# Performance work log

Hardware: AMD Instinct MI355X
Metric: run time of the kernel (lower is better)

Reference implementation:

```python
import jax, jax.numpy as jnp
import numpy as np

B, Tu, Tm, Tz = 32, 128, 128, 32
V, H, E = 10000, 512, 128
S = E + H  # state_size


def setup_inputs() -> dict:
    key = jax.random.key(0)
    ks = jax.random.split(key, 24)
    u_input = jax.random.randint(ks[0], (B, Tu), 0, V)
    m_input = jax.random.randint(ks[1], (B, Tm), 0, V)
    pv_z_idx = jax.random.randint(ks[2], (B, Tz), 0, V)
    inp = {
        'u_input': u_input,
        'u_input_1hot': jax.nn.one_hot(u_input, V, dtype=jnp.float32),
        'u_hiddens': jax.random.normal(ks[3], (B, Tu, H), jnp.float32),
        'm_input': m_input,
        'm_input_1hot': jax.nn.one_hot(m_input, V, dtype=jnp.float32),
        'm_hiddens': jax.random.normal(ks[4], (B, Tm, H), jnp.float32),
        'pv_z_prob': jax.nn.softmax(jax.random.normal(ks[5], (B, Tz, V), jnp.float32), axis=-1),
        'pv_z_hidden': jax.random.normal(ks[6], (B, Tz, H), jnp.float32),
        'pv_z_idx': pv_z_idx,
        'emb_zt': jax.random.normal(ks[7], (B, 1, E), jnp.float32),
        'last_hidden': jax.random.normal(ks[8], (1, B, H), jnp.float32),
        # Attn params (concat attention: v . tanh(W [h; enc]))
        'W_attn': jax.random.normal(ks[9], (H, 2 * H), jnp.float32) * 0.02,
        'b_attn': jnp.zeros((H,), jnp.float32),
        'v_attn': jax.random.normal(ks[10], (H,), jnp.float32) * 0.05,
        # GRU params (torch gate order r,z,n)
        'W_ih': jax.random.normal(ks[11], (3 * H, S), jnp.float32) * 0.02,
        'W_hh': jax.random.normal(ks[12], (3 * H, H), jnp.float32) * 0.02,
        'b_ih': jnp.zeros((3 * H,), jnp.float32),
        'b_hh': jnp.zeros((3 * H,), jnp.float32),
        # generation / copy-score projections
        'W_gen': jax.random.normal(ks[13], (V, S), jnp.float32) * 0.02,
        'b_gen': jnp.zeros((V,), jnp.float32),
        'W_cpu': jax.random.normal(ks[14], (S, H), jnp.float32) * 0.02,
        'b_cpu': jnp.zeros((S,), jnp.float32),
        'W_cpm': jax.random.normal(ks[15], (S, H), jnp.float32) * 0.02,
        'b_cpm': jnp.zeros((S,), jnp.float32),
        'W_cppz': jax.random.normal(ks[16], (S, H), jnp.float32) * 0.02,
        'b_cppz': jnp.zeros((S,), jnp.float32),
    }
    return inp


def reference(u_input, u_input_1hot, u_hiddens, m_input, m_input_1hot, m_hiddens,
              pv_z_prob, pv_z_hidden, pv_z_idx, emb_zt, last_hidden,
              W_attn, b_attn, v_attn, W_ih, W_hh, b_ih, b_hh,
              W_gen, b_gen, W_cpu, b_cpu, W_cpm, b_cpm, W_cppz, b_cppz):
    Bv, Tuv, Vv = u_input_1hot.shape
    Tmv = m_hiddens.shape[1]
    t_input = emb_zt  # [B,1,E] (enable_selc_read=False)

    # ---- concat attention over [u; m; pv_z] hiddens ----
    enc = jnp.concatenate([u_hiddens, m_hiddens, pv_z_hidden], axis=1)  # [B,T,H]
    h0 = jnp.transpose(last_hidden, (1, 0, 2))  # [B,1,H]
    hid_rep = jnp.broadcast_to(h0, (Bv, enc.shape[1], h0.shape[2]))
    energy = jnp.tanh(jnp.einsum('bth,gh->btg', jnp.concatenate([hid_rep, enc], axis=2), W_attn) + b_attn)
    attn_w = jax.nn.softmax(jnp.einsum('bth,h->bt', energy, v_attn), axis=1)
    context = jnp.einsum('bt,bth->bh', attn_w, enc)[:, None, :]  # [B,1,H]

    # ---- single GRU step (torch gate order r,z,n) ----
    x = jnp.concatenate([t_input, context], axis=2)[:, 0, :]  # [B,E+H]
    h = h0[:, 0, :]
    gi = x @ W_ih.T + b_ih
    gh = h @ W_hh.T + b_hh
    i_r, i_z, i_n = jnp.split(gi, 3, axis=1)
    h_r, h_z, h_n = jnp.split(gh, 3, axis=1)
    r = jax.nn.sigmoid(i_r + h_r)
    z = jax.nn.sigmoid(i_z + h_z)
    n = jnp.tanh(i_n + r * h_n)
    h_new = (1.0 - z) * n + z * h  # [B,H]
    gru_out = h_new[:, None, :]
    last_hidden_new = h_new[None, :, :]

    # ---- generation + copy scores ----
    st = jnp.concatenate([h_new, t_input[:, 0, :]], axis=1)  # [B,E+H]
    score_g = st @ W_gen.T + b_gen  # [B,V]
    sc_u = jnp.einsum('bts,bs->bt', jnp.tanh(jnp.einsum('bth,sh->bts', u_hiddens, W_cpu) + b_cpu), st)
    sc_m = jnp.einsum('bts,bs->bt', jnp.tanh(jnp.einsum('bth,sh->bts', m_hiddens, W_cpm) + b_cpm), st)
    sc_pz = jnp.einsum('bts,bs->bt', jnp.tanh(jnp.einsum('bth,sh->bts', pv_z_hidden, W_cppz) + b_cppz), st)
    probs = jax.nn.softmax(jnp.concatenate([score_g, sc_u, sc_m, sc_pz], axis=1), axis=1)

    p_g = probs[:, :Vv]
    p_u = probs[:, Vv:Vv + Tuv]
    p_m = probs[:, Vv + Tuv:Vv + Tuv + Tmv]
    p_pz = probs[:, Vv + Tuv + Tmv:]
    prob_out = (p_g
                + jnp.einsum('bt,btv->bv', p_u, u_input_1hot)
                + jnp.einsum('bt,btv->bv', p_m, m_input_1hot)
                + jnp.einsum('bt,btv->bv', p_pz, pv_z_prob))
    return (prob_out, last_hidden_new, gru_out)
```

## Files before the change

### kernel.cpp

```cpp
#include <hip/hip_runtime.h>
#include <math.h>

#define B   32
#define TU  128
#define TM  128
#define TZ  32
#define TENC 288
#define V   10000
#define H   512
#define E   128
#define S   640
#define G3  1536
#define NLOG (V + TENC)

#define WS_Q      0
#define WS_SCORE  (WS_Q + B*H)
#define WS_CTX    (WS_SCORE + B*TENC)
#define WS_GI     (WS_CTX + B*H)
#define WS_GH     (WS_GI + B*G3)
#define WS_ST     (WS_GH + B*G3)
#define WS_LOGIT  (WS_ST + B*S)
#define WS_PCOPY  (WS_LOGIT + B*NLOG)
#define WS_F_TOTAL (WS_PCOPY + B*TENC)

#define BF_WA2  0
#define BF_WCP  (BF_WA2 + 512*512)
#define BF_ENC  (BF_WCP + 3*640*512)
#define BF_ST   (BF_ENC + B*TENC*H)
#define BF_TANH (BF_ST + B*S)

typedef __attribute__((ext_vector_type(8))) short bf16x8_t;
typedef __attribute__((ext_vector_type(4))) float f32x4_t;
typedef __attribute__((ext_vector_type(16))) float f32x16_t;

__device__ __forceinline__ float fast_tanh(float x) {
    return 1.f - 2.f / (__expf(2.f * x) + 1.f);
}

__device__ __forceinline__ unsigned short f2bf(float x) {
    unsigned int u = __float_as_uint(x);
    u += 0x7fffu + ((u >> 16) & 1u);
    return (unsigned short)(u >> 16);
}

__device__ __forceinline__ float bf2f(unsigned short u) {
    return __uint_as_float(((unsigned int)u) << 16);
}

__device__ __forceinline__ bf16x8_t cvt8(const float* p) {
    float4 a = *(const float4*)(p);
    float4 b = *(const float4*)(p + 4);
    bf16x8_t r;
    r[0] = (short)f2bf(a.x); r[1] = (short)f2bf(a.y);
    r[2] = (short)f2bf(a.z); r[3] = (short)f2bf(a.w);
    r[4] = (short)f2bf(b.x); r[5] = (short)f2bf(b.y);
    r[6] = (short)f2bf(b.z); r[7] = (short)f2bf(b.w);
    return r;
}

__device__ __forceinline__ const float* enc_row(const float* u, const float* m,
                                                const float* pz, int b, int t) {
    if (t < TU) return u + ((size_t)b * TU + t) * H;
    if (t < TU + TM) return m + ((size_t)b * TM + (t - TU)) * H;
    return pz + ((size_t)b * TZ + (t - TU - TM)) * H;
}

#define CVT_WA2_END  65536
#define CVT_TOTAL    (CVT_WA2_END + 3*81920)
#define CVTE_TOTAL   (B * TENC * 128)
#define CVT_ALL      (CVT_TOTAL + CVTE_TOTAL)
#define NMV          112
__global__ __launch_bounds__(256) void k_prep(const float* __restrict__ W_attn,
                                              const float* __restrict__ W_cpu,
                                              const float* __restrict__ W_cpm,
                                              const float* __restrict__ W_cppz,
                                              const float* __restrict__ u_h,
                                              const float* __restrict__ m_h,
                                              const float* __restrict__ pz_h,
                                              const float* __restrict__ last_h,
                                              const float* __restrict__ emb,
                                              const float* __restrict__ W_hh,
                                              const float* __restrict__ W_ih,
                                              const float* __restrict__ b_attn,
                                              const float* __restrict__ b_hh,
                                              const float* __restrict__ b_ih,
                                              float* __restrict__ ws,
                                              unsigned short* __restrict__ bf) {
    int blk = blockIdx.x, tid = threadIdx.x;
    __shared__ float redmv[4][64][16];
    if (blk < NMV) {
        int wave = tid >> 6, lane = tid & 63;
        int m = lane & 31, khalf = lane >> 5;
        f32x16_t acc = {};
        int n;
        if (blk < 16) {
            n = blk * 32 + m;
            const float* aptr = last_h + (size_t)m * H + khalf * 8;
            const float* bptr = W_attn + (size_t)n * 1024 + khalf * 8;
            for (int k0 = wave * 128; k0 < wave * 128 + 128; k0 += 16)
                acc = __builtin_amdgcn_mfma_f32_32x32x16_bf16(cvt8(aptr + k0),
                                                              cvt8(bptr + k0), acc, 0, 0, 0);
        } else if (blk < 64) {
            n = (blk - 16) * 32 + m;
            const float* aptr = last_h + (size_t)m * H + khalf * 8;
            const float* bptr = W_hh + (size_t)n * H + khalf * 8;
            for (int k0 = wave * 128; k0 < wave * 128 + 128; k0 += 16)
                acc = __builtin_amdgcn_mfma_f32_32x32x16_bf16(cvt8(aptr + k0),
                                                              cvt8(bptr + k0), acc, 0, 0, 0);
        } else {
            n = (blk - 64) * 32 + m;
            const float* aptr = emb + (size_t)m * E + khalf * 8;
            const float* bptr = W_ih + (size_t)n * S + khalf * 8;
            for (int k0 = wave * 32; k0 < wave * 32 + 32; k0 += 16)
                acc = __builtin_amdgcn_mfma_f32_32x32x16_bf16(cvt8(aptr + k0),
                                                              cvt8(bptr + k0), acc, 0, 0, 0);
        }
#pragma unroll
        for (int r = 0; r < 16; ++r) redmv[wave][lane][r] = acc[r];
        __syncthreads();
        if (wave == 0) {
#pragma unroll
            for (int r = 0; r < 16; ++r) {
                float v = redmv[0][lane][r] + redmv[1][lane][r] +
                          redmv[2][lane][r] + redmv[3][lane][r];
                int row = (r & 3) + 8 * (r >> 2) + 4 * khalf;
                if (blk < 16)      ws[WS_Q  + row * H  + n] = v + b_attn[n];
                else if (blk < 64) ws[WS_GH + row * G3 + n] = v + b_hh[n];
                else               ws[WS_GI + row * G3 + n] = v + b_ih[n];
            }
        }
        return;
    }
    int idx = (blk - NMV) * 256 + tid;
    if (idx >= CVT_ALL) return;
    const float* src;
    unsigned short* dst;
    if (idx < CVT_WA2_END) {
        int g = idx >> 7, c4 = idx & 127;
        int k = c4 * 4, kt = k >> 5, kin = k & 31;
        src = W_attn + (size_t)g * 1024 + 512 + k;
        dst = bf + BF_WA2 + kt * (512 * 32) + g * 32 + kin;
    } else if (idx < CVT_TOTAL) {
        int r = idx - CVT_WA2_END;
        int seg = r / 81920, q = r % 81920;
        int s = q >> 7, c4 = q & 127;
        int k = c4 * 4, kt = k >> 5, kin = k & 31;
        const float* s0 = (seg == 0) ? W_cpu : (seg == 1) ? W_cpm : W_cppz;
        src = s0 + (size_t)s * 512 + k;
        dst = bf + BF_WCP + seg * 327680 + kt * (640 * 32) + s * 32 + kin;
    } else {
        int e = idx - CVT_TOTAL;
        int b = e / (TENC * 128);
        int r = e % (TENC * 128);
        int t = r >> 7, c4 = r & 127;
        int k = c4 * 4, kt = k >> 5, kin = k & 31;
        src = enc_row(u_h, m_h, pz_h, b, t) + k;
        dst = bf + BF_ENC + (((size_t)b * 16 + kt) * TENC + t) * 32 + kin;
    }
    float4 v = *(const float4*)src;
    ushort4 o;
    o.x = f2bf(v.x); o.y = f2bf(v.y); o.z = f2bf(v.z); o.w = f2bf(v.w);
    *(ushort4*)dst = o;
}

__global__ __launch_bounds__(256) void k_enc_mfma(const unsigned short* __restrict__ bf,
                                                  const float* __restrict__ v_attn,
                                                  const float* __restrict__ b_cpu,
                                                  const float* __restrict__ b_cpm,
                                                  const float* __restrict__ b_cppz,
                                                  float* __restrict__ ws,
                                                  unsigned short* __restrict__ bft) {
    __shared__ __attribute__((aligned(16))) unsigned short lds_w[640 * 32];
    __shared__ __attribute__((aligned(16))) unsigned short lds_a[32 * 32];
    __shared__ float red[4][32];
    int blk = blockIdx.x;
    int typeC = (blk >= 288);
    int idx = typeC ? blk - 288 : blk;
    int b = idx / 9, t0 = (idx % 9) * 32;
    int tid = threadIdx.x, wave = tid >> 6, lane = tid & 63;
    int n16 = lane & 15, quad = lane >> 4;
    const unsigned short* asrc0 =
        bf + BF_ENC + (((size_t)b * 16) * TENC + t0) * 32;
    if (!typeC) {
        f32x4_t acc[2][8];
#pragma unroll
        for (int tl = 0; tl < 2; ++tl)
#pragma unroll
            for (int j = 0; j < 8; ++j) acc[tl][j] = (f32x4_t){0.f, 0.f, 0.f, 0.f};
        for (int kt = 0; kt < 16; ++kt) {
            const unsigned short* wsrc = bf + BF_WA2 + (size_t)kt * (512 * 32);
#pragma unroll
            for (int c = 0; c < 8; ++c) {
                int u = (c * 256 + tid) * 8;
                *(bf16x8_t*)&lds_w[u] = *(const bf16x8_t*)&wsrc[u];
            }
            if (tid < 128) {
                int u = tid * 8;
                *(bf16x8_t*)&lds_a[u] =
                    *(const bf16x8_t*)&asrc0[(size_t)kt * TENC * 32 + u];
            }
            __syncthreads();
            bf16x8_t a0 = *(const bf16x8_t*)&lds_a[n16 * 32 + quad * 8];
            bf16x8_t a1 = *(const bf16x8_t*)&lds_a[(n16 + 16) * 32 + quad * 8];
#pragma unroll
            for (int j = 0; j < 8; ++j) {
                bf16x8_t bb = *(const bf16x8_t*)
                    &lds_w[((wave * 8 + j) * 16 + n16) * 32 + quad * 8];
                acc[0][j] = __builtin_amdgcn_mfma_f32_16x16x32_bf16(a0, bb, acc[0][j], 0, 0, 0);
                acc[1][j] = __builtin_amdgcn_mfma_f32_16x16x32_bf16(a1, bb, acc[1][j], 0, 0, 0);
            }
            __syncthreads();
        }
        float sval[2][4] = {{0.f, 0.f, 0.f, 0.f}, {0.f, 0.f, 0.f, 0.f}};
#pragma unroll
        for (int j = 0; j < 8; ++j) {
            int g = (wave * 8 + j) * 16 + n16;
            float q = ws[WS_Q + b * H + g];
            float va = v_attn[g];
#pragma unroll
            for (int tl = 0; tl < 2; ++tl)
#pragma unroll
                for (int r = 0; r < 4; ++r)
                    sval[tl][r] += fast_tanh(acc[tl][j][r] + q) * va;
        }
#pragma unroll
        for (int tl = 0; tl < 2; ++tl)
#pragma unroll
            for (int r = 0; r < 4; ++r)
#pragma unroll
                for (int off = 8; off > 0; off >>= 1)
                    sval[tl][r] += __shfl_down(sval[tl][r], off, 64);
        if (n16 == 0)
#pragma unroll
            for (int tl = 0; tl < 2; ++tl)
#pragma unroll
                for (int r = 0; r < 4; ++r)
                    red[wave][tl * 16 + quad * 4 + r] = sval[tl][r];
        __syncthreads();
        if (tid < 32)
            ws[WS_SCORE + b * TENC + t0 + tid] =
                red[0][tid] + red[1][tid] + red[2][tid] + red[3][tid];
    } else {
        int seg = (t0 < TU) ? 0 : (t0 < TU + TM) ? 1 : 2;
        const float* bias = (seg == 0) ? b_cpu : (seg == 1) ? b_cpm : b_cppz;
        f32x4_t acc[2][10];
#pragma unroll
        for (int tl = 0; tl < 2; ++tl)
#pragma unroll
            for (int j = 0; j < 10; ++j) acc[tl][j] = (f32x4_t){0.f, 0.f, 0.f, 0.f};
        for (int kt = 0; kt < 16; ++kt) {
            const unsigned short* wsrc =
                bf + BF_WCP + seg * 327680 + (size_t)kt * (640 * 32);
#pragma unroll
            for (int c = 0; c < 10; ++c) {
                int u = (c * 256 + tid) * 8;
                *(bf16x8_t*)&lds_w[u] = *(const bf16x8_t*)&wsrc[u];
            }
            if (tid < 128) {
                int u = tid * 8;
                *(bf16x8_t*)&lds_a[u] =
                    *(const bf16x8_t*)&asrc0[(size_t)kt * TENC * 32 + u];
            }
            __syncthreads();
            bf16x8_t a0 = *(const bf16x8_t*)&lds_a[n16 * 32 + quad * 8];
            bf16x8_t a1 = *(const bf16x8_t*)&lds_a[(n16 + 16) * 32 + quad * 8];
#pragma unroll
            for (int j = 0; j < 10; ++j) {
                bf16x8_t bb = *(const bf16x8_t*)
                    &lds_w[((wave * 10 + j) * 16 + n16) * 32 + quad * 8];
                acc[0][j] = __builtin_amdgcn_mfma_f32_16x16x32_bf16(a0, bb, acc[0][j], 0, 0, 0);
                acc[1][j] = __builtin_amdgcn_mfma_f32_16x16x32_bf16(a1, bb, acc[1][j], 0, 0, 0);
            }
            __syncthreads();
        }
#pragma unroll
        for (int j = 0; j < 10; ++j) {
            int s = (wave * 10 + j) * 16 + n16;
            float bi = bias[s];
#pragma unroll
            for (int tl = 0; tl < 2; ++tl)
#pragma unroll
                for (int r = 0; r < 4; ++r) {
                    int t = t0 + tl * 16 + quad * 4 + r;
                    bft[BF_TANH + ((size_t)b * TENC + t) * S + s] =
                        f2bf(fast_tanh(acc[tl][j][r] + bi));
                }
        }
    }
}

__global__ __launch_bounds__(256) void k_softmax_ctx(const unsigned short* __restrict__ bf,
                                                     float* __restrict__ ws) {
    int b = blockIdx.x, tid = threadIdx.x;
    __shared__ float wsm[TENC];
    __shared__ float red1[4], red2[4];
    float local = -1e30f;
    for (int t = tid; t < TENC; t += 256) {
        float s = ws[WS_SCORE + b * TENC + t];
        wsm[t] = s;
        local = fmaxf(local, s);
    }
    int lane = tid & 63, wv = tid >> 6;
    for (int off = 32; off > 0; off >>= 1) local = fmaxf(local, __shfl_down(local, off, 64));
    if (lane == 0) red1[wv] = local;
    __syncthreads();
    float mx = fmaxf(fmaxf(red1[0], red1[1]), fmaxf(red1[2], red1[3]));
    float ls = 0.f;
    for (int t = tid; t < TENC; t += 256) {
        float e = __expf(wsm[t] - mx);
        wsm[t] = e;
        ls += e;
    }
    for (int off = 32; off > 0; off >>= 1) ls += __shfl_down(ls, off, 64);
    if (lane == 0) red2[wv] = ls;
    __syncthreads();
    float inv = 1.f / (red2[0] + red2[1] + red2[2] + red2[3]);

    int h2 = tid * 2;
    int kt = h2 >> 5, hin = h2 & 31;
    const unsigned short* ep = bf + BF_ENC + ((size_t)b * 16 + kt) * TENC * 32 + hin;
    float a00 = 0.f, a01 = 0.f, a10 = 0.f, a11 = 0.f;
#pragma unroll 2
    for (int t = 0; t < TENC; t += 2) {
        ushort2 v0 = *(const ushort2*)(ep + (size_t)t * 32);
        ushort2 v1 = *(const ushort2*)(ep + (size_t)(t + 1) * 32);
        float w0 = wsm[t], w1 = wsm[t + 1];
        a00 += w0 * bf2f(v0.x); a10 += w0 * bf2f(v0.y);
        a01 += w1 * bf2f(v1.x); a11 += w1 * bf2f(v1.y);
    }
    ws[WS_CTX + b * H + h2]     = (a00 + a01) * inv;
    ws[WS_CTX + b * H + h2 + 1] = (a10 + a11) * inv;
}

__global__ __launch_bounds__(256) void k_gru_ctx(const float* __restrict__ W_ih,
                                                 float* __restrict__ ws) {
    int blk = blockIdx.x, tid = threadIdx.x;
    __shared__ float redmv[4][64][16];
    int wave = tid >> 6, lane = tid & 63;
    int m = lane & 31, khalf = lane >> 5;
    int n = blk * 32 + m;
    const float* aptr = ws + WS_CTX + (size_t)m * H + khalf * 8;
    const float* bptr = W_ih + (size_t)n * S + E + khalf * 8;
    f32x16_t acc = {};
    for (int k0 = wave * 128; k0 < wave * 128 + 128; k0 += 16)
        acc = __builtin_amdgcn_mfma_f32_32x32x16_bf16(cvt8(aptr + k0),
                                                      cvt8(bptr + k0), acc, 0, 0, 0);
#pragma unroll
    for (int r = 0; r < 16; ++r) redmv[wave][lane][r] = acc[r];
    __syncthreads();
    if (wave == 0) {
#pragma unroll
        for (int r = 0; r < 16; ++r) {
            float v = redmv[0][lane][r] + redmv[1][lane][r] +
                      redmv[2][lane][r] + redmv[3][lane][r];
            int row = (r & 3) + 8 * (r >> 2) + 4 * khalf;
            ws[WS_GI + row * G3 + n] += v;
        }
    }
}

__global__ __launch_bounds__(256) void k_combine(const float* __restrict__ emb,
                                                 const float* __restrict__ last_hidden,
                                                 float* __restrict__ ws,
                                                 unsigned short* __restrict__ bf,
                                                 float* __restrict__ out) {
    int i = blockIdx.x * 256 + threadIdx.x;
    int b = i >> 9, h = i & 511;
    float gi_r = ws[WS_GI + b * G3 + h];
    float gi_z = ws[WS_GI + b * G3 + H + h];
    float gi_n = ws[WS_GI + b * G3 + 2 * H + h];
    float gh_r = ws[WS_GH + b * G3 + h];
    float gh_z = ws[WS_GH + b * G3 + H + h];
    float gh_n = ws[WS_GH + b * G3 + 2 * H + h];
    float rr = 1.f / (1.f + __expf(-(gi_r + gh_r)));
    float zz = 1.f / (1.f + __expf(-(gi_z + gh_z)));
    float nn = fast_tanh(gi_n + rr * gh_n);
    float hp = last_hidden[b * H + h];
    float hn = (1.f - zz) * nn + zz * hp;
    out[V * B + b * H + h] = hn;
    out[V * B + B * H + b * H + h] = hn;
    ws[WS_ST + b * S + h] = hn;
    bf[BF_ST + b * S + h] = f2bf(hn);
    if (h < E) {
        float ev = emb[b * E + h];
        ws[WS_ST + b * S + H + h] = ev;
        bf[BF_ST + b * S + H + h] = f2bf(ev);
    }
}

__global__ __launch_bounds__(256) void k_logits(const unsigned short* __restrict__ bf,
                                                const float* __restrict__ W_gen,
                                                const float* __restrict__ b_gen,
                                                float* __restrict__ ws) {
    int blk = blockIdx.x, tid = threadIdx.x;
    __shared__ float shmem[4 * 64 * 16];
    int wave = tid >> 6, lane = tid & 63;
    if (blk < 576) {
        int b = blk / 18, t0 = (blk % 18) * 16;
        float* st_s = shmem;
        for (int i = tid; i < S; i += 256) st_s[i] = ws[WS_ST + b * S + i];
        __syncthreads();
#pragma unroll
        for (int tl = 0; tl < 4; ++tl) {
            int t = t0 + wave * 4 + tl;
            const unsigned short* row = bf + BF_TANH + ((size_t)b * TENC + t) * S;
            float acc = 0.f;
#pragma unroll
            for (int i = 0; i < 10; ++i) {
                int s = lane + 64 * i;
                acc += bf2f(row[s]) * st_s[s];
            }
            for (int off = 32; off > 0; off >>= 1) acc += __shfl_down(acc, off, 64);
            if (lane == 0) ws[WS_LOGIT + (size_t)b * NLOG + V + t] = acc;
        }
    } else {
        float (*redmv)[64][16] = (float (*)[64][16])shmem;
        int m = lane & 31, khalf = lane >> 5;
        int n = (blk - 576) * 32 + m;
        int nr = (n < V) ? n : (V - 1);
        const unsigned short* aptr = bf + BF_ST + (size_t)m * S + khalf * 8;
        const float* bptr = W_gen + (size_t)nr * S + khalf * 8;
        f32x16_t acc = {};
        for (int k0 = wave * 160; k0 < wave * 160 + 160; k0 += 16)
            acc = __builtin_amdgcn_mfma_f32_32x32x16_bf16(*(const bf16x8_t*)(aptr + k0),
                                                          cvt8(bptr + k0), acc, 0, 0, 0);
#pragma unroll
        for (int r = 0; r < 16; ++r) redmv[wave][lane][r] = acc[r];
        __syncthreads();
        if (wave == 0 && n < V) {
            float bg = b_gen[n];
#pragma unroll
            for (int r = 0; r < 16; ++r) {
                float v = redmv[0][lane][r] + redmv[1][lane][r] +
                          redmv[2][lane][r] + redmv[3][lane][r];
                int row = (r & 3) + 8 * (r >> 2) + 4 * khalf;
                ws[WS_LOGIT + (size_t)row * NLOG + n] = v + bg;
            }
        }
    }
}

__global__ __launch_bounds__(512) void k_softmax_scatter(const int* __restrict__ u_in,
                                                         const int* __restrict__ m_in,
                                                         float* __restrict__ ws,
                                                         float* __restrict__ out) {
    int b = blockIdx.x, tid = threadIdx.x;
    __shared__ float red1[8], red2[8];
    __shared__ float ex[NLOG];
    const float* lg = ws + WS_LOGIT + (size_t)b * NLOG;
    float mx = -1e30f;
    for (int i = tid; i < NLOG; i += 512) {
        float v = lg[i];
        ex[i] = v;
        mx = fmaxf(mx, v);
    }
    int lane = tid & 63, wv = tid >> 6;
    for (int off = 32; off > 0; off >>= 1) mx = fmaxf(mx, __shfl_down(mx, off, 64));
    if (lane == 0) red1[wv] = mx;
    __syncthreads();
    mx = red1[0];
#pragma unroll
    for (int w = 1; w < 8; ++w) mx = fmaxf(mx, red1[w]);
    float sm = 0.f;
    for (int i = tid; i < NLOG; i += 512) {
        float e = __expf(ex[i] - mx);
        ex[i] = e;
        sm += e;
    }
    for (int off = 32; off > 0; off >>= 1) sm += __shfl_down(sm, off, 64);
    if (lane == 0) red2[wv] = sm;
    __syncthreads();
    sm = red2[0];
#pragma unroll
    for (int w = 1; w < 8; ++w) sm += red2[w];
    float inv = 1.f / sm;
    for (int i = tid; i < V; i += 512) out[b * V + i] = ex[i] * inv;
    __syncthreads();
    if (tid < TU + TM) {
        int idx = (tid < TU) ? u_in[b * TU + tid] : m_in[b * TM + (tid - TU)];
        atomicAdd(&out[(size_t)b * V + idx], ex[V + tid] * inv);
    } else if (tid < TENC) {
        ws[WS_PCOPY + b * TENC + tid] = ex[V + tid] * inv;
    }
}

__global__ __launch_bounds__(256) void k_pv(const float* __restrict__ pvp,
                                            const float* __restrict__ ws,
                                            float* __restrict__ out) {
    int b = blockIdx.y;
    int v = blockIdx.x * 256 + threadIdx.x;
    __shared__ float p[TZ];
    if (threadIdx.x < TZ) p[threadIdx.x] = ws[WS_PCOPY + b * TENC + TU + TM + threadIdx.x];
    __syncthreads();
    if (v >= V) return;
    float acc = 0.f;
#pragma unroll 4
    for (int t = 0; t < TZ; ++t) acc += p[t] * pvp[((size_t)b * TZ + t) * V + v];
    out[(size_t)b * V + v] += acc;
}

extern "C" void kernel_launch(void* const* d_in, const int* in_sizes, int n_in,
                              void* d_out, int out_size, void* d_ws, size_t ws_size,
                              hipStream_t stream) {
    const int*   u_input   = (const int*)d_in[0];
    const float* u_h       = (const float*)d_in[2];
    const int*   m_input   = (const int*)d_in[3];
    const float* m_h       = (const float*)d_in[5];
    const float* pv_prob   = (const float*)d_in[6];
    const float* pz_h      = (const float*)d_in[7];
    const float* emb       = (const float*)d_in[9];
    const float* last_h    = (const float*)d_in[10];
    const float* W_attn    = (const float*)d_in[11];
    const float* b_attn    = (const float*)d_in[12];
    const float* v_attn    = (const float*)d_in[13];
    const float* W_ih      = (const float*)d_in[14];
    const float* W_hh      = (const float*)d_in[15];
    const float* b_ih      = (const float*)d_in[16];
    const float* b_hh      = (const float*)d_in[17];
    const float* W_gen     = (const float*)d_in[18];
    const float* b_gen     = (const float*)d_in[19];
    const float* W_cpu     = (const float*)d_in[20];
    const float* b_cpu     = (const float*)d_in[21];
    const float* W_cpm     = (const float*)d_in[22];
    const float* b_cpm     = (const float*)d_in[23];
    const float* W_cppz    = (const float*)d_in[24];
    const float* b_cppz    = (const float*)d_in[25];
    float* ws  = (float*)d_ws;
    unsigned short* bf = (unsigned short*)(ws + WS_F_TOTAL);
    float* out = (float*)d_out;

    hipLaunchKernelGGL(k_prep, dim3(NMV + CVT_ALL / 256), dim3(256), 0, stream,
                       W_attn, W_cpu, W_cpm, W_cppz, u_h, m_h, pz_h,
                       last_h, emb, W_hh, W_ih, b_attn, b_hh, b_ih, ws, bf);
    hipLaunchKernelGGL(k_enc_mfma, dim3(576), dim3(256), 0, stream,
                       bf, v_attn, b_cpu, b_cpm, b_cppz, ws, bf);
    hipLaunchKernelGGL(k_softmax_ctx, dim3(B), dim3(256), 0, stream, bf, ws);
    hipLaunchKernelGGL(k_gru_ctx, dim3(48), dim3(256), 0, stream, W_ih, ws);
    hipLaunchKernelGGL(k_combine, dim3(64), dim3(256), 0, stream, emb, last_h, ws, bf, out);
    hipLaunchKernelGGL(k_logits, dim3(576 + 313), dim3(256), 0, stream, bf, W_gen, b_gen, ws);
    hipLaunchKernelGGL(k_softmax_scatter, dim3(B), dim3(512), 0, stream,
                       u_input, m_input, ws, out);
    hipLaunchKernelGGL(k_pv, dim3(40, B), dim3(256), 0, stream, pv_prob, ws, out);
}
```

Before: 468.1 us.

## Register-prefetch next K-tile in attention/copy GEMM and unroll pv loop more

```diff
diff --git a/kernel.cpp b/kernel.cpp
--- a/kernel.cpp
+++ b/kernel.cpp
@@ -182,24 +182,46 @@
     const unsigned short* asrc0 =
         bf + BF_ENC + (((size_t)b * 16) * TENC + t0) * 32;
     if (!typeC) {
+        bf16x8_t rw0, rw1, rw2, rw3, rw4, rw5, rw6, rw7, ra;
+        const unsigned short* wb = bf + BF_WA2;
+        rw0 = *(const bf16x8_t*)&wb[(0 * 256 + tid) * 8];
+        rw1 = *(const bf16x8_t*)&wb[(1 * 256 + tid) * 8];
+        rw2 = *(const bf16x8_t*)&wb[(2 * 256 + tid) * 8];
+        rw3 = *(const bf16x8_t*)&wb[(3 * 256 + tid) * 8];
+        rw4 = *(const bf16x8_t*)&wb[(4 * 256 + tid) * 8];
+        rw5 = *(const bf16x8_t*)&wb[(5 * 256 + tid) * 8];
+        rw6 = *(const bf16x8_t*)&wb[(6 * 256 + tid) * 8];
+        rw7 = *(const bf16x8_t*)&wb[(7 * 256 + tid) * 8];
+        if (tid < 128) ra = *(const bf16x8_t*)&asrc0[tid * 8];
+        *(bf16x8_t*)&lds_w[(0 * 256 + tid) * 8] = rw0;
+        *(bf16x8_t*)&lds_w[(1 * 256 + tid) * 8] = rw1;
+        *(bf16x8_t*)&lds_w[(2 * 256 + tid) * 8] = rw2;
+        *(bf16x8_t*)&lds_w[(3 * 256 + tid) * 8] = rw3;
+        *(bf16x8_t*)&lds_w[(4 * 256 + tid) * 8] = rw4;
+        *(bf16x8_t*)&lds_w[(5 * 256 + tid) * 8] = rw5;
+        *(bf16x8_t*)&lds_w[(6 * 256 + tid) * 8] = rw6;
+        *(bf16x8_t*)&lds_w[(7 * 256 + tid) * 8] = rw7;
+        if (tid < 128) *(bf16x8_t*)&lds_a[tid * 8] = ra;
+        __syncthreads();
         f32x4_t acc[2][8];
 #pragma unroll
         for (int tl = 0; tl < 2; ++tl)
 #pragma unroll
             for (int j = 0; j < 8; ++j) acc[tl][j] = (f32x4_t){0.f, 0.f, 0.f, 0.f};
         for (int kt = 0; kt < 16; ++kt) {
-            const unsigned short* wsrc = bf + BF_WA2 + (size_t)kt * (512 * 32);
-#pragma unroll
-            for (int c = 0; c < 8; ++c) {
-                int u = (c * 256 + tid) * 8;
-                *(bf16x8_t*)&lds_w[u] = *(const bf16x8_t*)&wsrc[u];
-            }
-            if (tid < 128) {
-                int u = tid * 8;
-                *(bf16x8_t*)&lds_a[u] =
-                    *(const bf16x8_t*)&asrc0[(size_t)kt * TENC * 32 + u];
-            }
-            __syncthreads();
+            if (kt < 15) {
+                const unsigned short* wsrc = wb + (size_t)(kt + 1) * (512 * 32);
+                rw0 = *(const bf16x8_t*)&wsrc[(0 * 256 + tid) * 8];
+                rw1 = *(const bf16x8_t*)&wsrc[(1 * 256 + tid) * 8];
+                rw2 = *(const bf16x8_t*)&wsrc[(2 * 256 + tid) * 8];
+                rw3 = *(const bf16x8_t*)&wsrc[(3 * 256 + tid) * 8];
+                rw4 = *(const bf16x8_t*)&wsrc[(4 * 256 + tid) * 8];
+                rw5 = *(const bf16x8_t*)&wsrc[(5 * 256 + tid) * 8];
+                rw6 = *(const bf16x8_t*)&wsrc[(6 * 256 + tid) * 8];
+                rw7 = *(const bf16x8_t*)&wsrc[(7 * 256 + tid) * 8];
+                if (tid < 128)
+                    ra = *(const bf16x8_t*)&asrc0[(size_t)(kt + 1) * TENC * 32 + tid * 8];
+            }
             bf16x8_t a0 = *(const bf16x8_t*)&lds_a[n16 * 32 + quad * 8];
             bf16x8_t a1 = *(const bf16x8_t*)&lds_a[(n16 + 16) * 32 + quad * 8];
 #pragma unroll
@@ -208,6 +230,18 @@
                     &lds_w[((wave * 8 + j) * 16 + n16) * 32 + quad * 8];
                 acc[0][j] = __builtin_amdgcn_mfma_f32_16x16x32_bf16(a0, bb, acc[0][j], 0, 0, 0);
                 acc[1][j] = __builtin_amdgcn_mfma_f32_16x16x32_bf16(a1, bb, acc[1][j], 0, 0, 0);
+            }
+            __syncthreads();
+            if (kt < 15) {
+                *(bf16x8_t*)&lds_w[(0 * 256 + tid) * 8] = rw0;
+                *(bf16x8_t*)&lds_w[(1 * 256 + tid) * 8] = rw1;
+                *(bf16x8_t*)&lds_w[(2 * 256 + tid) * 8] = rw2;
+                *(bf16x8_t*)&lds_w[(3 * 256 + tid) * 8] = rw3;
+                *(bf16x8_t*)&lds_w[(4 * 256 + tid) * 8] = rw4;
+                *(bf16x8_t*)&lds_w[(5 * 256 + tid) * 8] = rw5;
+                *(bf16x8_t*)&lds_w[(6 * 256 + tid) * 8] = rw6;
+                *(bf16x8_t*)&lds_w[(7 * 256 + tid) * 8] = rw7;
+                if (tid < 128) *(bf16x8_t*)&lds_a[tid * 8] = ra;
             }
             __syncthreads();
         }
@@ -243,25 +277,52 @@
     } else {
         int seg = (t0 < TU) ? 0 : (t0 < TU + TM) ? 1 : 2;
         const float* bias = (seg == 0) ? b_cpu : (seg == 1) ? b_cpm : b_cppz;
+        const unsigned short* wb = bf + BF_WCP + seg * 327680;
+        bf16x8_t rw0, rw1, rw2, rw3, rw4, rw5, rw6, rw7, rw8, rw9, ra;
+        rw0 = *(const bf16x8_t*)&wb[(0 * 256 + tid) * 8];
+        rw1 = *(const bf16x8_t*)&wb[(1 * 256 + tid) * 8];
+        rw2 = *(const bf16x8_t*)&wb[(2 * 256 + tid) * 8];
+        rw3 = *(const bf16x8_t*)&wb[(3 * 256 + tid) * 8];
+        rw4 = *(const bf16x8_t*)&wb[(4 * 256 + tid) * 8];
+        rw5 = *(const bf16x8_t*)&wb[(5 * 256 + tid) * 8];
+        rw6 = *(const bf16x8_t*)&wb[(6 * 256 + tid) * 8];
+        rw7 = *(const bf16x8_t*)&wb[(7 * 256 + tid) * 8];
+        rw8 = *(const bf16x8_t*)&wb[(8 * 256 + tid) * 8];
+        rw9 = *(const bf16x8_t*)&wb[(9 * 256 + tid) * 8];
+        if (tid < 128) ra = *(const bf16x8_t*)&asrc0[tid * 8];
+        *(bf16x8_t*)&lds_w[(0 * 256 + tid) * 8] = rw0;
+        *(bf16x8_t*)&lds_w[(1 * 256 + tid) * 8] = rw1;
+        *(bf16x8_t*)&lds_w[(2 * 256 + tid) * 8] = rw2;
+        *(bf16x8_t*)&lds_w[(3 * 256 + tid) * 8] = rw3;
+        *(bf16x8_t*)&lds_w[(4 * 256 + tid) * 8] = rw4;
+        *(bf16x8_t*)&lds_w[(5 * 256 + tid) * 8] = rw5;
+        *(bf16x8_t*)&lds_w[(6 * 256 + tid) * 8] = rw6;
+        *(bf16x8_t*)&lds_w[(7 * 256 + tid) * 8] = rw7;
+        *(bf16x8_t*)&lds_w[(8 * 256 + tid) * 8] = rw8;
+        *(bf16x8_t*)&lds_w[(9 * 256 + tid) * 8] = rw9;
+        if (tid < 128) *(bf16x8_t*)&lds_a[tid * 8] = ra;
+        __syncthreads();
         f32x4_t acc[2][10];
 #pragma unroll
         for (int tl = 0; tl < 2; ++tl)
 #pragma unroll
             for (int j = 0; j < 10; ++j) acc[tl][j] = (f32x4_t){0.f, 0.f, 0.f, 0.f};
         for (int kt = 0; kt < 16; ++kt) {
-            const unsigned short* wsrc =
-                bf + BF_WCP + seg * 327680 + (size_t)kt * (640 * 32);
-#pragma unroll
-            for (int c = 0; c < 10; ++c) {
-                int u = (c * 256 + tid) * 8;
-                *(bf16x8_t*)&lds_w[u] = *(const bf16x8_t*)&wsrc[u];
-            }
-            if (tid < 128) {
-                int u = tid * 8;
-                *(bf16x8_t*)&lds_a[u] =
-                    *(const bf16x8_t*)&asrc0[(size_t)kt * TENC * 32 + u];
-            }
-            __syncthreads();
+            if (kt < 15) {
+                const unsigned short* wsrc = wb + (size_t)(kt + 1) * (640 * 32);
+                rw0 = *(const bf16x8_t*)&wsrc[(0 * 256 + tid) * 8];
+                rw1 = *(const bf16x8_t*)&wsrc[(1 * 256 + tid) * 8];
+                rw2 = *(const bf16x8_t*)&wsrc[(2 * 256 + tid) * 8];
+                rw3 = *(const bf16x8_t*)&wsrc[(3 * 256 + tid) * 8];
+                rw4 = *(const bf16x8_t*)&wsrc[(4 * 256 + tid) * 8];
+                rw5 = *(const bf16x8_t*)&wsrc[(5 * 256 + tid) * 8];
+                rw6 = *(const bf16x8_t*)&wsrc[(6 * 256 + tid) * 8];
+                rw7 = *(const bf16x8_t*)&wsrc[(7 * 256 + tid) * 8];
+                rw8 = *(const bf16x8_t*)&wsrc[(8 * 256 + tid) * 8];
+                rw9 = *(const bf16x8_t*)&wsrc[(9 * 256 + tid) * 8];
+                if (tid < 128)
+                    ra = *(const bf16x8_t*)&asrc0[(size_t)(kt + 1) * TENC * 32 + tid * 8];
+            }
             bf16x8_t a0 = *(const bf16x8_t*)&lds_a[n16 * 32 + quad * 8];
             bf16x8_t a1 = *(const bf16x8_t*)&lds_a[(n16 + 16) * 32 + quad * 8];
 #pragma unroll
@@ -270,6 +331,20 @@
                     &lds_w[((wave * 10 + j) * 16 + n16) * 32 + quad * 8];
                 acc[0][j] = __builtin_amdgcn_mfma_f32_16x16x32_bf16(a0, bb, acc[0][j], 0, 0, 0);
                 acc[1][j] = __builtin_amdgcn_mfma_f32_16x16x32_bf16(a1, bb, acc[1][j], 0, 0, 0);
+            }
+            __syncthreads();
+            if (kt < 15) {
+                *(bf16x8_t*)&lds_w[(0 * 256 + tid) * 8] = rw0;
+                *(bf16x8_t*)&lds_w[(1 * 256 + tid) * 8] = rw1;
+                *(bf16x8_t*)&lds_w[(2 * 256 + tid) * 8] = rw2;
+                *(bf16x8_t*)&lds_w[(3 * 256 + tid) * 8] = rw3;
+                *(bf16x8_t*)&lds_w[(4 * 256 + tid) * 8] = rw4;
+                *(bf16x8_t*)&lds_w[(5 * 256 + tid) * 8] = rw5;
+                *(bf16x8_t*)&lds_w[(6 * 256 + tid) * 8] = rw6;
+                *(bf16x8_t*)&lds_w[(7 * 256 + tid) * 8] = rw7;
+                *(bf16x8_t*)&lds_w[(8 * 256 + tid) * 8] = rw8;
+                *(bf16x8_t*)&lds_w[(9 * 256 + tid) * 8] = rw9;
+                if (tid < 128) *(bf16x8_t*)&lds_a[tid * 8] = ra;
             }
             __syncthreads();
         }
@@ -494,7 +569,7 @@
     __syncthreads();
     if (v >= V) return;
     float acc = 0.f;
-#pragma unroll 4
+#pragma unroll 8
     for (int t = 0; t < TZ; ++t) acc += p[t] * pvp[((size_t)b * TZ + t) * V + v];
     out[(size_t)b * V + v] += acc;
 }
```

After: 455.2 us. -2.7%, faster.
